# Performance work log

Hardware: AMD Instinct MI355X
Metric: run time of the kernel (lower is better)

The kernel has to match this reference:

```python
import jax, jax.numpy as jnp
import numpy as np

# Standard 2D morphsnakes structuring elements (4 line filters), matching the
# repo-level global `filters` used by LSNet2.
_SE = np.zeros((4, 3, 3), dtype=np.float32)
_SE[0, 1, :] = 1.0           # horizontal line
_SE[1, :, 1] = 1.0           # vertical line
_SE[2] = np.eye(3, dtype=np.float32)          # main diagonal
_SE[3] = np.eye(3, dtype=np.float32)[::-1]    # anti-diagonal


def _dilate_stack(x, filts):
    # per-pixel: max over 3x3 window of (zero-padded x + filt), for every filter
    H, W = x.shape
    p = jnp.pad(x, 1)
    m = jnp.full((filts.shape[0], H, W), -jnp.inf, x.dtype)
    for k in range(3):
        for l in range(3):
            m = jnp.maximum(m, p[k:k + H, l:l + W][None] + filts[:, k, l][:, None, None])
    return m  # [F, H, W]


def _erode_stack(x, filts):
    # per-pixel: min over 3x3 window of (zero-padded x - filt) == -max(-(x - filt))
    H, W = x.shape
    p = jnp.pad(x, 1)
    m = jnp.full((filts.shape[0], H, W), jnp.inf, x.dtype)
    for k in range(3):
        for l in range(3):
            m = jnp.minimum(m, p[k:k + H, l:l + W][None] - filts[:, k, l][:, None, None])
    return m  # [F, H, W]


def _dilate_min(x, filts):
    return jnp.min(_dilate_stack(x, filts), axis=0)


def _erode_max(x, filts):
    return jnp.max(_erode_stack(x, filts), axis=0)


def setup_inputs() -> dict:
    key = jax.random.key(0)
    k1, k2 = jax.random.split(key)
    H = W = 2048
    inp = jax.random.uniform(k1, (H, W), dtype=jnp.float32)
    origin = jax.random.uniform(k2, (H, W), dtype=jnp.float32)
    filters = jnp.asarray(_SE)
    return {"input": inp, "origin": origin, "filters": filters}


def reference(input, origin, filters):
    x = input
    # SI o IS smoothing: dilate/min, erode/max, erode/max, dilate/min, dilate/min, erode/max
    x = _dilate_min(x, filters)
    x = _erode_max(x, filters)
    x = _erode_max(x, filters)
    x = _dilate_min(x, filters)
    x = _dilate_min(x, filters)
    x = _erode_max(x, filters)

    # balloon force with v = 1 and a flat ones(3,3) structuring element
    ones_f = jnp.ones((1, 3, 3), x.dtype)
    aux = _dilate_stack(x, ones_f)[0]
    threshold = jnp.percentile(x, 40.0)
    x = jnp.where(origin > threshold, aux, x)

    # Chan-Vese region means and update
    c0 = jnp.sum(origin * (1.0 - x)) / (jnp.sum(1.0 - x) + 1e-8)
    c1 = jnp.sum(origin * x) / (jnp.sum(x) + 1e-8)
    cv = (origin - c1) ** 2 - (origin - c0) ** 2
    x = jnp.where(cv < 0, 1.0, jnp.where(cv > 0, 0.0, x))
    return x
```

## Files before the change

### kernel.cpp

```cpp
#include <hip/hip_runtime.h>

#define HH 2048
#define WW 2048
#define NN (HH*WW)

static constexpr unsigned RANK0 = 1677721u;
static constexpr unsigned KEYLO = 0xB000u;
static constexpr unsigned KEYHI_ = 0xC000u;
static constexpr int NBINS = 4096;
static constexpr int NPART = 512;

#define TH 32
#define TW 128
#define LR 44
#define LCP 148

struct Scal {
  unsigned keyhiA, keyhiB, rA, rB;
  double thr, c0, c1;
};

static constexpr size_t OFF_CTL    = (size_t)NN * 4;
static constexpr size_t OFF_COARSE = OFF_CTL;
static constexpr size_t OFF_UNDER  = OFF_COARSE + (size_t)NBINS * 4;
static constexpr size_t OFF_OVER   = OFF_UNDER + 4;
static constexpr size_t OFF_MIDA   = OFF_OVER + 4;
static constexpr size_t OFF_MIDB   = OFF_MIDA + 1024;
static constexpr size_t OFF_H2A    = OFF_MIDB + 1024;
static constexpr size_t OFF_H2B    = OFF_H2A + 65536ull * 4;
static constexpr size_t CTL_END    = OFF_H2B + 65536ull * 4;
static constexpr size_t CTL_BYTES  = CTL_END - OFF_CTL;
static constexpr size_t OFF_SCAL   = CTL_END;
static constexpr size_t OFF_PART   = OFF_SCAL + 64;

__device__ __forceinline__ float mx3(float a, float b, float c){ return fmaxf(fmaxf(a,b),c); }
__device__ __forceinline__ float mn3(float a, float b, float c){ return fminf(fminf(a,b),c); }

__device__ __forceinline__ unsigned keyf(float x){
  unsigned b = __float_as_uint(x);
  return (b & 0x80000000u) ? ~b : (b | 0x80000000u);
}
__device__ __forceinline__ float keyinv(unsigned k){
  unsigned b = (k & 0x80000000u) ? (k ^ 0x80000000u) : ~k;
  return __uint_as_float(b);
}

__device__ __forceinline__ void loadwin6(const float* __restrict__ src, int rowbase,
                                         int cL, int cC, int cR, float w[6]){
  float4 v = *reinterpret_cast<const float4*>(&src[rowbase + cC]);
  w[0] = src[rowbase + cL];
  w[1]=v.x; w[2]=v.y; w[3]=v.z; w[4]=v.w;
  w[5] = src[rowbase + cR];
}

__device__ __forceinline__ void morph4(bool DIL,
    const float pr[6], const float cr[6], const float nr[6], float w[4]){
  #pragma unroll
  for (int i = 0; i < 4; i++){
    if (DIL){
      float Ah = mx3(cr[i],   cr[i+1], cr[i+2]);
      float Av = mx3(pr[i+1], cr[i+1], nr[i+1]);
      float Ad = mx3(pr[i],   cr[i+1], nr[i+2]);
      float Aa = mx3(pr[i+2], cr[i+1], nr[i]);
      float tm = mx3(pr[i], pr[i+1], pr[i+2]);
      float bm = mx3(nr[i], nr[i+1], nr[i+2]);
      float M9 = mx3(tm, Ah, bm);
      w[i] = fmaxf(M9, 1.0f + fminf(fminf(Ah,Av), fminf(Ad,Aa)));
    } else {
      float Bh = mn3(cr[i],   cr[i+1], cr[i+2]);
      float Bv = mn3(pr[i+1], cr[i+1], nr[i+1]);
      float Bd = mn3(pr[i],   cr[i+1], nr[i+2]);
      float Ba = mn3(pr[i+2], cr[i+1], nr[i]);
      float tm = mn3(pr[i], pr[i+1], pr[i+2]);
      float bm = mn3(nr[i], nr[i+1], nr[i+2]);
      float m9 = mn3(tm, Bh, bm);
      w[i] = fminf(m9, fmaxf(fmaxf(Bh,Bv), fmaxf(Bd,Ba)) - 1.0f);
    }
  }
}

__global__ __launch_bounds__(256)
void fused_morph_k(const float* __restrict__ in, float* __restrict__ out,
                   unsigned* __restrict__ gh, unsigned* __restrict__ under,
                   unsigned* __restrict__ over){
  __shared__ float lds[2][LR*LCP];
  const int tilec = blockIdx.x & 15;
  const int tiler = blockIdx.x >> 4;
  const int r0 = tiler*TH, c0 = tilec*TW;

  for (int idx = threadIdx.x; idx < LR*36; idx += 256){
    int lr = idx / 36, g = idx % 36;
    int gr = r0 - 6 + lr, gc = c0 - 8 + 4*g;
    float4 v = make_float4(0.f,0.f,0.f,0.f);
    if ((unsigned)gr < (unsigned)HH && (unsigned)gc < (unsigned)WW)
      v = *reinterpret_cast<const float4*>(in + (size_t)gr*WW + gc);
    *reinterpret_cast<float4*>(&lds[0][lr*LCP + 4*g]) = v;
  }
  __syncthreads();

  const int t = threadIdx.x;
  const int g = t % 36, s = t / 36;
  const bool active = (t < 252);
  const int colC = 4*g;
  const int colL = g ? 4*g - 1 : 0;
  const int colR = (g == 35) ? 143 : 4*g + 4;
  const int gcBase = c0 - 8 + 4*g;
  const bool dilf[6] = {true,false,false,true,true,false};

  #pragma unroll 1
  for (int st = 0; st < 6; st++){
    const float* src = lds[st & 1];
    float*       dst = lds[(st & 1) ^ 1];
    if (active){
      const bool DIL = dilf[st];
      float r8[8][6];
      #pragma unroll
      for (int k = 0; k < 8; k++)
        loadwin6(src, (6*s + k)*LCP, colL, colC, colR, r8[k]);
      #pragma unroll
      for (int k = 0; k < 6; k++){
        float w[4];
        morph4(DIL, r8[k], r8[k+1], r8[k+2], w);
        int gr = r0 - 6 + 6*s + 1 + k;
        if ((unsigned)gr >= (unsigned)HH){
          w[0]=w[1]=w[2]=w[3]=0.f;
        } else {
          #pragma unroll
          for (int i = 0; i < 4; i++)
            if ((unsigned)(gcBase + i) >= (unsigned)WW) w[i] = 0.f;
        }
        *reinterpret_cast<float4*>(&dst[(6*s + 1 + k)*LCP + colC]) =
            make_float4(w[0],w[1],w[2],w[3]);
      }
    }
    __syncthreads();
  }
  unsigned* lh = reinterpret_cast<unsigned*>(&lds[1][0]);
  for (int i = threadIdx.x; i < NBINS; i += 256) lh[i] = 0;
  __syncthreads();

  unsigned uc = 0, oc = 0;
  for (int idx = threadIdx.x; idx < TH*(TW/4); idx += 256){
    int row = idx >> 5, gg = idx & 31;
    float4 v = *reinterpret_cast<const float4*>(&lds[0][(row+6)*LCP + 8 + 4*gg]);
    *reinterpret_cast<float4*>(out + (size_t)(r0+row)*WW + c0 + 4*gg) = v;
    float vv[4] = {v.x, v.y, v.z, v.w};
    #pragma unroll
    for (int i = 0; i < 4; i++){
      unsigned key = keyf(vv[i]);
      unsigned hi = key >> 16;
      if (hi >= KEYLO && hi < KEYHI_) atomicAdd(&lh[hi - KEYLO], 1u);
      else if (hi < KEYLO)            uc++;
      else                            oc++;
    }
  }
  __syncthreads();
  for (int i = threadIdx.x; i < NBINS; i += 256){
    unsigned c = lh[i];
    if (c) atomicAdd(&gh[i], c);
  }
  if (uc) atomicAdd(under, uc);
  if (oc) atomicAdd(over, oc);
}

__global__ void scan_coarse_k(const unsigned* __restrict__ gh, const unsigned* __restrict__ under,
                              Scal* __restrict__ sc){
  __shared__ unsigned part[256];
  __shared__ unsigned excl[256];
  int t = threadIdx.x;
  unsigned loc = 0;
  #pragma unroll
  for (int i = 0; i < NBINS/256; i++) loc += gh[t*(NBINS/256) + i];
  part[t] = loc;
  __syncthreads();
  if (t == 0){
    unsigned run = under[0];
    for (int i = 0; i < 256; i++){ excl[i] = run; run += part[i]; }
  }
  __syncthreads();
  unsigned run = excl[t];
  const unsigned r0 = RANK0, r1 = RANK0 + 1;
  #pragma unroll
  for (int i = 0; i < NBINS/256; i++){
    unsigned idx = t*(NBINS/256) + i;
    unsigned cc = gh[idx];
    if (cc){
      if (r0 >= run && r0 - run < cc){ sc->keyhiA = KEYLO + idx; sc->rA = r0 - run; }
      if (r1 >= run && r1 - run < cc){ sc->keyhiB = KEYLO + idx; sc->rB = r1 - run; }
    }
    run += cc;
  }
}

__global__ __launch_bounds__(256)
void fine2d_k(const float* __restrict__ x, const Scal* __restrict__ sc,
              unsigned* __restrict__ midA, unsigned* __restrict__ midB,
              unsigned* __restrict__ h2A, unsigned* __restrict__ h2B){
  __shared__ unsigned hA[256], hB[256];
  hA[threadIdx.x] = 0; hB[threadIdx.x] = 0;
  __syncthreads();
  unsigned ha = sc->keyhiA, hb = sc->keyhiB;
  bool dup = (ha == hb);
  const int nItems = NN/4;
  for (int it = blockIdx.x*blockDim.x + threadIdx.x; it < nItems; it += gridDim.x*blockDim.x){
    float4 v = reinterpret_cast<const float4*>(x)[it];
    float vv[4] = {v.x, v.y, v.z, v.w};
    #pragma unroll
    for (int j = 0; j < 4; j++){
      unsigned key = keyf(vv[j]);
      unsigned hi = key >> 16;
      if (hi == ha){ atomicAdd(&hA[(key>>8)&255], 1u); atomicAdd(&h2A[key & 0xFFFFu], 1u); }
      else if (hi == hb){ atomicAdd(&hB[(key>>8)&255], 1u); atomicAdd(&h2B[key & 0xFFFFu], 1u); }
    }
  }
  __syncthreads();
  if (hA[threadIdx.x]) atomicAdd(&midA[threadIdx.x], hA[threadIdx.x]);
  if (!dup && hB[threadIdx.x]) atomicAdd(&midB[threadIdx.x], hB[threadIdx.x]);
}

__global__ void scan_ml_k(const unsigned* __restrict__ midA, const unsigned* __restrict__ midB,
                          const unsigned* __restrict__ h2A, const unsigned* __restrict__ h2B,
                          Scal* __restrict__ sc){
  __shared__ unsigned h[256], excl[256];
  __shared__ unsigned res[6];
  int t = threadIdx.x;
  unsigned ha = sc->keyhiA, hb = sc->keyhiB;
  bool dupHi = (ha == hb);
  unsigned rA = sc->rA, rB = sc->rB;

  h[t] = midA[t];
  __syncthreads();
  if (t == 0){ unsigned run = 0; for (int i = 0; i < 256; i++){ excl[i] = run; run += h[i]; } }
  __syncthreads();
  if (rA >= excl[t] && rA - excl[t] < h[t]){ res[0] = (unsigned)t; res[1] = rA - excl[t]; }
  if (dupHi && rB >= excl[t] && rB - excl[t] < h[t]){ res[2] = (unsigned)t; res[3] = rB - excl[t]; }
  __syncthreads();
  if (!dupHi){
    h[t] = midB[t];
    __syncthreads();
    if (t == 0){ unsigned run = 0; for (int i = 0; i < 256; i++){ excl[i] = run; run += h[i]; } }
    __syncthreads();
    if (rB >= excl[t] && rB - excl[t] < h[t]){ res[2] = (unsigned)t; res[3] = rB - excl[t]; }
    __syncthreads();
  }
  unsigned mA = res[0], rA2 = res[1], mB = res[2], rB2 = res[3];
  bool dupMid = dupHi && (mA == mB);

  h[t] = h2A[mA*256 + t];
  __syncthreads();
  if (t == 0){ unsigned run = 0; for (int i = 0; i < 256; i++){ excl[i] = run; run += h[i]; } }
  __syncthreads();
  if (rA2 >= excl[t] && rA2 - excl[t] < h[t]) res[4] = (unsigned)t;
  if (dupMid && rB2 >= excl[t] && rB2 - excl[t] < h[t]) res[5] = (unsigned)t;
  __syncthreads();
  if (!dupMid){
    const unsigned* srcH = dupHi ? h2A : h2B;
    h[t] = srcH[mB*256 + t];
    __syncthreads();
    if (t == 0){ unsigned run = 0; for (int i = 0; i < 256; i++){ excl[i] = run; run += h[i]; } }
    __syncthreads();
    if (rB2 >= excl[t] && rB2 - excl[t] < h[t]) res[5] = (unsigned)t;
    __syncthreads();
  }
  if (t == 0){
    unsigned ka = (ha << 16) | (mA << 8) | res[4];
    unsigned kb = (hb << 16) | (mB << 8) | res[5];
    double va = (double)keyinv(ka), vb = (double)keyinv(kb);
    const double FRAC = 0.4*(double)(NN-1) - (double)RANK0;
    sc->thr = va + (vb - va) * FRAC;
  }
}

__device__ __forceinline__ void load6(const float* __restrict__ p, int row, int q, float r[6]){
  if (row < 0 || row >= HH){
    r[0]=r[1]=r[2]=r[3]=r[4]=r[5]=0.f;
    return;
  }
  const float* rp = p + (size_t)row * WW;
  float4 cc = *reinterpret_cast<const float4*>(rp + q);
  r[0] = (q > 0) ? rp[q-1] : 0.f;
  r[1]=cc.x; r[2]=cc.y; r[3]=cc.z; r[4]=cc.w;
  r[5] = (q+4 < WW) ? rp[q+4] : 0.f;
}

__global__ __launch_bounds__(256)
void balloon_k(const float* __restrict__ x, const float* __restrict__ orig,
               float* __restrict__ xb, const Scal* __restrict__ sc, double* __restrict__ part){
  double thr = sc->thr;
  double s0 = 0.0, s1 = 0.0, s2 = 0.0;
  const int nItems = NN/4;
  for (int it = blockIdx.x*blockDim.x + threadIdx.x; it < nItems; it += gridDim.x*blockDim.x){
    int i = it >> 9;
    int q = (it & 511) << 2;
    float a[6], b[6], c[6];
    load6(x, i-1, q, a);
    load6(x, i,   q, b);
    load6(x, i+1, q, c);
    float4 og = *reinterpret_cast<const float4*>(orig + (size_t)i*WW + q);
    float ov[4] = {og.x, og.y, og.z, og.w};
    float r[4];
    #pragma unroll
    for (int t = 0; t < 4; t++){
      float M9 = mx3(mx3(a[t],a[t+1],a[t+2]), mx3(b[t],b[t+1],b[t+2]), mx3(c[t],c[t+1],c[t+2]));
      float aux = 1.0f + M9;
      float nx = ((double)ov[t] > thr) ? aux : b[t+1];
      r[t] = nx;
      s0 += (double)ov[t];
      s1 += (double)nx;
      s2 += (double)ov[t] * (double)nx;
    }
    *reinterpret_cast<float4*>(xb + (size_t)i*WW + q) = make_float4(r[0],r[1],r[2],r[3]);
  }
  for (int off = 32; off > 0; off >>= 1){
    s0 += __shfl_down(s0, off);
    s1 += __shfl_down(s1, off);
    s2 += __shfl_down(s2, off);
  }
  __shared__ double red[4][3];
  int lane = threadIdx.x & 63, wv = threadIdx.x >> 6;
  if (lane == 0){ red[wv][0] = s0; red[wv][1] = s1; red[wv][2] = s2; }
  __syncthreads();
  if (threadIdx.x == 0){
    part[blockIdx.x*3+0] = red[0][0]+red[1][0]+red[2][0]+red[3][0];
    part[blockIdx.x*3+1] = red[0][1]+red[1][1]+red[2][1]+red[3][1];
    part[blockIdx.x*3+2] = red[0][2]+red[1][2]+red[2][2]+red[3][2];
  }
}

__global__ void c0c1_k(const double* __restrict__ part, Scal* __restrict__ sc){
  int t = threadIdx.x;
  double s0 = 0, s1 = 0, s2 = 0;
  for (int b = t; b < NPART; b += 256){
    s0 += part[b*3+0]; s1 += part[b*3+1]; s2 += part[b*3+2];
  }
  for (int off = 32; off > 0; off >>= 1){
    s0 += __shfl_down(s0, off);
    s1 += __shfl_down(s1, off);
    s2 += __shfl_down(s2, off);
  }
  __shared__ double red[4][3];
  int lane = t & 63, wv = t >> 6;
  if (lane == 0){ red[wv][0] = s0; red[wv][1] = s1; red[wv][2] = s2; }
  __syncthreads();
  if (t == 0){
    double So = red[0][0]+red[1][0]+red[2][0]+red[3][0];
    double Sx = red[0][1]+red[1][1]+red[2][1]+red[3][1];
    double Sox= red[0][2]+red[1][2]+red[2][2]+red[3][2];
    sc->c0 = (So - Sox) / ((double)NN - Sx + 1e-8);
    sc->c1 = Sox / (Sx + 1e-8);
  }
}

__global__ __launch_bounds__(256)
void final_k(const float* __restrict__ orig, const float* __restrict__ xb,
             const Scal* __restrict__ sc, float* __restrict__ out){
  double c0 = sc->c0, c1 = sc->c1;
  const int nItems = NN/4;
  for (int it = blockIdx.x*blockDim.x + threadIdx.x; it < nItems; it += gridDim.x*blockDim.x){
    float4 og = reinterpret_cast<const float4*>(orig)[it];
    float4 xv = reinterpret_cast<const float4*>(xb)[it];
    float ov[4] = {og.x, og.y, og.z, og.w};
    float xx[4] = {xv.x, xv.y, xv.z, xv.w};
    float r[4];
    #pragma unroll
    for (int t = 0; t < 4; t++){
      double o = (double)ov[t];
      double d1 = o - c1, d0 = o - c0;
      double cv = d1*d1 - d0*d0;
      r[t] = (cv < 0.0) ? 1.0f : ((cv > 0.0) ? 0.0f : xx[t]);
    }
    reinterpret_cast<float4*>(out)[it] = make_float4(r[0],r[1],r[2],r[3]);
  }
}

extern "C" void kernel_launch(void* const* d_in, const int* in_sizes, int n_in,
                              void* d_out, int out_size, void* d_ws, size_t ws_size,
                              hipStream_t stream) {
  const float* input  = (const float*)d_in[0];
  const float* origin = (const float*)d_in[1];
  float* out = (float*)d_out;

  char* ws = (char*)d_ws;
  float*    bufA   = (float*)ws;
  unsigned* coarse = (unsigned*)(ws + OFF_COARSE);
  unsigned* under  = (unsigned*)(ws + OFF_UNDER);
  unsigned* over   = (unsigned*)(ws + OFF_OVER);
  unsigned* midA   = (unsigned*)(ws + OFF_MIDA);
  unsigned* midB   = (unsigned*)(ws + OFF_MIDB);
  unsigned* h2A    = (unsigned*)(ws + OFF_H2A);
  unsigned* h2B    = (unsigned*)(ws + OFF_H2B);
  Scal*     scal   = (Scal*)(ws + OFF_SCAL);
  double*   part   = (double*)(ws + OFF_PART);

  hipMemsetAsync(ws + OFF_CTL, 0, CTL_BYTES, stream);

  fused_morph_k<<<(HH/TH)*(WW/TW), 256, 0, stream>>>(input, out, coarse, under, over);

  scan_coarse_k<<<1, 256, 0, stream>>>(coarse, under, scal);
  fine2d_k<<<1024, 256, 0, stream>>>(out, scal, midA, midB, h2A, h2B);
  scan_ml_k<<<1, 256, 0, stream>>>(midA, midB, h2A, h2B, scal);

  balloon_k<<<NPART, 256, 0, stream>>>(out, origin, bufA, scal, part);
  c0c1_k<<<1, 256, 0, stream>>>(part, scal);
  final_k<<<2048, 256, 0, stream>>>(origin, bufA, scal, out);
}
```

Baseline: 118.6 us.

## Fold single-block scan kernels into consumers with redundant per-block rank selection

Removes the three single-block kernels (coarse scan, mid/low-level rank scan, c0/c1 reduction) by having every block of the consuming kernel recompute them redundantly, using a warp-shuffle exclusive scan instead of a serial thread-0 scan. This cuts the launch count from seven to four and drops the serialized tiny-kernel latency between passes. In exchange, each block repeats the histogram scans and partial-sum reduction, adding global reads and syncs per block. Grid sizes for the fine-histogram and balloon passes are also raised to 2048 blocks.

```diff
diff --git a/kernel.cpp b/kernel.cpp
--- a/kernel.cpp
+++ b/kernel.cpp
@@ -8,17 +8,12 @@
 static constexpr unsigned KEYLO = 0xB000u;
 static constexpr unsigned KEYHI_ = 0xC000u;
 static constexpr int NBINS = 4096;
-static constexpr int NPART = 512;
+static constexpr int NPART = 2048;
 
 #define TH 32
 #define TW 128
 #define LR 44
 #define LCP 148
-
-struct Scal {
-  unsigned keyhiA, keyhiB, rA, rB;
-  double thr, c0, c1;
-};
 
 static constexpr size_t OFF_CTL    = (size_t)NN * 4;
 static constexpr size_t OFF_COARSE = OFF_CTL;
@@ -30,8 +25,7 @@
 static constexpr size_t OFF_H2B    = OFF_H2A + 65536ull * 4;
 static constexpr size_t CTL_END    = OFF_H2B + 65536ull * 4;
 static constexpr size_t CTL_BYTES  = CTL_END - OFF_CTL;
-static constexpr size_t OFF_SCAL   = CTL_END;
-static constexpr size_t OFF_PART   = OFF_SCAL + 64;
+static constexpr size_t OFF_PART   = CTL_END;
 
 __device__ __forceinline__ float mx3(float a, float b, float c){ return fmaxf(fmaxf(a,b),c); }
 __device__ __forceinline__ float mn3(float a, float b, float c){ return fminf(fminf(a,b),c); }
@@ -43,6 +37,50 @@
 __device__ __forceinline__ float keyinv(unsigned k){
   unsigned b = (k & 0x80000000u) ? (k ^ 0x80000000u) : ~k;
   return __uint_as_float(b);
+}
+
+__device__ __forceinline__ unsigned excl_scan256(unsigned v, volatile unsigned* tmp, int t){
+  int lane = t & 63, wv = t >> 6;
+  unsigned inc = v;
+  #pragma unroll
+  for (int off = 1; off < 64; off <<= 1){
+    unsigned u = __shfl_up(inc, off);
+    if (lane >= off) inc += u;
+  }
+  if (lane == 63) tmp[wv] = inc;
+  __syncthreads();
+  unsigned wo = 0;
+  #pragma unroll
+  for (int w = 0; w < 4; w++) wo += (w < wv) ? tmp[w] : 0u;
+  __syncthreads();
+  return wo + inc - v;
+}
+
+__device__ __forceinline__ void coarse_rank(const unsigned* __restrict__ gh,
+                                            const unsigned* __restrict__ under,
+                                            unsigned* cres, volatile unsigned* stmp, int t){
+  unsigned bins[16], loc = 0;
+  #pragma unroll
+  for (int i = 0; i < 16; i++){ bins[i] = gh[t*16 + i]; loc += bins[i]; }
+  unsigned run = excl_scan256(loc, stmp, t) + under[0];
+  #pragma unroll
+  for (int i = 0; i < 16; i++){
+    unsigned cc = bins[i];
+    if (cc){
+      if (RANK0 >= run && RANK0 - run < cc){ cres[0] = KEYLO + (unsigned)(t*16+i); cres[1] = RANK0 - run; }
+      if (RANK0+1 >= run && RANK0+1 - run < cc){ cres[2] = KEYLO + (unsigned)(t*16+i); cres[3] = RANK0+1 - run; }
+    }
+    run += cc;
+  }
+  __syncthreads();
+}
+
+__device__ __forceinline__ void rank256(const unsigned* __restrict__ h, unsigned r,
+                                        unsigned* res2, volatile unsigned* stmp, int t){
+  unsigned c = h[t];
+  unsigned ex = excl_scan256(c, stmp, t);
+  if (c && r >= ex && r - ex < c){ res2[0] = (unsigned)t; res2[1] = r - ex; }
+  __syncthreads();
 }
 
 __device__ __forceinline__ void loadwin6(const float* __restrict__ src, int rowbase,
@@ -163,46 +201,21 @@
   if (oc) atomicAdd(over, oc);
 }
 
-__global__ void scan_coarse_k(const unsigned* __restrict__ gh, const unsigned* __restrict__ under,
-                              Scal* __restrict__ sc){
-  __shared__ unsigned part[256];
-  __shared__ unsigned excl[256];
-  int t = threadIdx.x;
-  unsigned loc = 0;
-  #pragma unroll
-  for (int i = 0; i < NBINS/256; i++) loc += gh[t*(NBINS/256) + i];
-  part[t] = loc;
-  __syncthreads();
-  if (t == 0){
-    unsigned run = under[0];
-    for (int i = 0; i < 256; i++){ excl[i] = run; run += part[i]; }
-  }
-  __syncthreads();
-  unsigned run = excl[t];
-  const unsigned r0 = RANK0, r1 = RANK0 + 1;
-  #pragma unroll
-  for (int i = 0; i < NBINS/256; i++){
-    unsigned idx = t*(NBINS/256) + i;
-    unsigned cc = gh[idx];
-    if (cc){
-      if (r0 >= run && r0 - run < cc){ sc->keyhiA = KEYLO + idx; sc->rA = r0 - run; }
-      if (r1 >= run && r1 - run < cc){ sc->keyhiB = KEYLO + idx; sc->rB = r1 - run; }
-    }
-    run += cc;
-  }
-}
-
 __global__ __launch_bounds__(256)
-void fine2d_k(const float* __restrict__ x, const Scal* __restrict__ sc,
+void fine2d_k(const float* __restrict__ x,
+              const unsigned* __restrict__ coarse, const unsigned* __restrict__ under,
               unsigned* __restrict__ midA, unsigned* __restrict__ midB,
               unsigned* __restrict__ h2A, unsigned* __restrict__ h2B){
   __shared__ unsigned hA[256], hB[256];
-  hA[threadIdx.x] = 0; hB[threadIdx.x] = 0;
-  __syncthreads();
-  unsigned ha = sc->keyhiA, hb = sc->keyhiB;
+  __shared__ unsigned stmp[4], cres[4];
+  const int t = threadIdx.x;
+  coarse_rank(coarse, under, cres, stmp, t);
+  unsigned ha = cres[0], hb = cres[2];
   bool dup = (ha == hb);
+  hA[t] = 0; hB[t] = 0;
+  __syncthreads();
   const int nItems = NN/4;
-  for (int it = blockIdx.x*blockDim.x + threadIdx.x; it < nItems; it += gridDim.x*blockDim.x){
+  for (int it = blockIdx.x*blockDim.x + t; it < nItems; it += gridDim.x*blockDim.x){
     float4 v = reinterpret_cast<const float4*>(x)[it];
     float vv[4] = {v.x, v.y, v.z, v.w};
     #pragma unroll
@@ -214,61 +227,8 @@
     }
   }
   __syncthreads();
-  if (hA[threadIdx.x]) atomicAdd(&midA[threadIdx.x], hA[threadIdx.x]);
-  if (!dup && hB[threadIdx.x]) atomicAdd(&midB[threadIdx.x], hB[threadIdx.x]);
-}
-
-__global__ void scan_ml_k(const unsigned* __restrict__ midA, const unsigned* __restrict__ midB,
-                          const unsigned* __restrict__ h2A, const unsigned* __restrict__ h2B,
-                          Scal* __restrict__ sc){
-  __shared__ unsigned h[256], excl[256];
-  __shared__ unsigned res[6];
-  int t = threadIdx.x;
-  unsigned ha = sc->keyhiA, hb = sc->keyhiB;
-  bool dupHi = (ha == hb);
-  unsigned rA = sc->rA, rB = sc->rB;
-
-  h[t] = midA[t];
-  __syncthreads();
-  if (t == 0){ unsigned run = 0; for (int i = 0; i < 256; i++){ excl[i] = run; run += h[i]; } }
-  __syncthreads();
-  if (rA >= excl[t] && rA - excl[t] < h[t]){ res[0] = (unsigned)t; res[1] = rA - excl[t]; }
-  if (dupHi && rB >= excl[t] && rB - excl[t] < h[t]){ res[2] = (unsigned)t; res[3] = rB - excl[t]; }
-  __syncthreads();
-  if (!dupHi){
-    h[t] = midB[t];
-    __syncthreads();
-    if (t == 0){ unsigned run = 0; for (int i = 0; i < 256; i++){ excl[i] = run; run += h[i]; } }
-    __syncthreads();
-    if (rB >= excl[t] && rB - excl[t] < h[t]){ res[2] = (unsigned)t; res[3] = rB - excl[t]; }
-    __syncthreads();
-  }
-  unsigned mA = res[0], rA2 = res[1], mB = res[2], rB2 = res[3];
-  bool dupMid = dupHi && (mA == mB);
-
-  h[t] = h2A[mA*256 + t];
-  __syncthreads();
-  if (t == 0){ unsigned run = 0; for (int i = 0; i < 256; i++){ excl[i] = run; run += h[i]; } }
-  __syncthreads();
-  if (rA2 >= excl[t] && rA2 - excl[t] < h[t]) res[4] = (unsigned)t;
-  if (dupMid && rB2 >= excl[t] && rB2 - excl[t] < h[t]) res[5] = (unsigned)t;
-  __syncthreads();
-  if (!dupMid){
-    const unsigned* srcH = dupHi ? h2A : h2B;
-    h[t] = srcH[mB*256 + t];
-    __syncthreads();
-    if (t == 0){ unsigned run = 0; for (int i = 0; i < 256; i++){ excl[i] = run; run += h[i]; } }
-    __syncthreads();
-    if (rB2 >= excl[t] && rB2 - excl[t] < h[t]) res[5] = (unsigned)t;
-    __syncthreads();
-  }
-  if (t == 0){
-    unsigned ka = (ha << 16) | (mA << 8) | res[4];
-    unsigned kb = (hb << 16) | (mB << 8) | res[5];
-    double va = (double)keyinv(ka), vb = (double)keyinv(kb);
-    const double FRAC = 0.4*(double)(NN-1) - (double)RANK0;
-    sc->thr = va + (vb - va) * FRAC;
-  }
+  if (hA[t]) atomicAdd(&midA[t], hA[t]);
+  if (!dup && hB[t]) atomicAdd(&midB[t], hB[t]);
 }
 
 __device__ __forceinline__ void load6(const float* __restrict__ p, int row, int q, float r[6]){
@@ -285,11 +245,32 @@
 
 __global__ __launch_bounds__(256)
 void balloon_k(const float* __restrict__ x, const float* __restrict__ orig,
-               float* __restrict__ xb, const Scal* __restrict__ sc, double* __restrict__ part){
-  double thr = sc->thr;
+               float* __restrict__ xb,
+               const unsigned* __restrict__ coarse, const unsigned* __restrict__ under,
+               const unsigned* __restrict__ midA, const unsigned* __restrict__ midB,
+               const unsigned* __restrict__ h2A, const unsigned* __restrict__ h2B,
+               double* __restrict__ part){
+  __shared__ unsigned stmp[4], cres[4], mresA[2], mresB[2], lresA[2], lresB[2];
+  __shared__ double red[4][3];
+  const int t = threadIdx.x;
+
+  coarse_rank(coarse, under, cres, stmp, t);
+  unsigned ha = cres[0], rA = cres[1], hb = cres[2], rB = cres[3];
+  bool dupHi = (ha == hb);
+  rank256(midA, rA, mresA, stmp, t);
+  rank256(dupHi ? midA : midB, rB, mresB, stmp, t);
+  unsigned mA = mresA[0], rA2 = mresA[1], mB = mresB[0], rB2 = mresB[1];
+  rank256(h2A + (size_t)mA*256, rA2, lresA, stmp, t);
+  rank256((dupHi ? h2A : h2B) + (size_t)mB*256, rB2, lresB, stmp, t);
+  unsigned ka = (ha << 16) | (mA << 8) | lresA[0];
+  unsigned kb = (hb << 16) | (mB << 8) | lresB[0];
+  double va = (double)keyinv(ka), vb = (double)keyinv(kb);
+  const double FRAC = 0.4*(double)(NN-1) - (double)RANK0;
+  double thr = va + (vb - va) * FRAC;
+
   double s0 = 0.0, s1 = 0.0, s2 = 0.0;
   const int nItems = NN/4;
-  for (int it = blockIdx.x*blockDim.x + threadIdx.x; it < nItems; it += gridDim.x*blockDim.x){
+  for (int it = blockIdx.x*blockDim.x + t; it < nItems; it += gridDim.x*blockDim.x){
     int i = it >> 9;
     int q = (it & 511) << 2;
     float a[6], b[6], c[6];
@@ -300,14 +281,14 @@
     float ov[4] = {og.x, og.y, og.z, og.w};
     float r[4];
     #pragma unroll
-    for (int t = 0; t < 4; t++){
-      float M9 = mx3(mx3(a[t],a[t+1],a[t+2]), mx3(b[t],b[t+1],b[t+2]), mx3(c[t],c[t+1],c[t+2]));
+    for (int j = 0; j < 4; j++){
+      float M9 = mx3(mx3(a[j],a[j+1],a[j+2]), mx3(b[j],b[j+1],b[j+2]), mx3(c[j],c[j+1],c[j+2]));
       float aux = 1.0f + M9;
-      float nx = ((double)ov[t] > thr) ? aux : b[t+1];
-      r[t] = nx;
-      s0 += (double)ov[t];
+      float nx = ((double)ov[j] > thr) ? aux : b[j+1];
+      r[j] = nx;
+      s0 += (double)ov[j];
       s1 += (double)nx;
-      s2 += (double)ov[t] * (double)nx;
+      s2 += (double)ov[j] * (double)nx;
     }
     *reinterpret_cast<float4*>(xb + (size_t)i*WW + q) = make_float4(r[0],r[1],r[2],r[3]);
   }
@@ -316,58 +297,58 @@
     s1 += __shfl_down(s1, off);
     s2 += __shfl_down(s2, off);
   }
-  __shared__ double red[4][3];
-  int lane = threadIdx.x & 63, wv = threadIdx.x >> 6;
+  int lane = t & 63, wv = t >> 6;
   if (lane == 0){ red[wv][0] = s0; red[wv][1] = s1; red[wv][2] = s2; }
   __syncthreads();
-  if (threadIdx.x == 0){
+  if (t == 0){
     part[blockIdx.x*3+0] = red[0][0]+red[1][0]+red[2][0]+red[3][0];
     part[blockIdx.x*3+1] = red[0][1]+red[1][1]+red[2][1]+red[3][1];
     part[blockIdx.x*3+2] = red[0][2]+red[1][2]+red[2][2]+red[3][2];
   }
 }
 
-__global__ void c0c1_k(const double* __restrict__ part, Scal* __restrict__ sc){
-  int t = threadIdx.x;
-  double s0 = 0, s1 = 0, s2 = 0;
-  for (int b = t; b < NPART; b += 256){
-    s0 += part[b*3+0]; s1 += part[b*3+1]; s2 += part[b*3+2];
-  }
-  for (int off = 32; off > 0; off >>= 1){
-    s0 += __shfl_down(s0, off);
-    s1 += __shfl_down(s1, off);
-    s2 += __shfl_down(s2, off);
-  }
-  __shared__ double red[4][3];
-  int lane = t & 63, wv = t >> 6;
-  if (lane == 0){ red[wv][0] = s0; red[wv][1] = s1; red[wv][2] = s2; }
-  __syncthreads();
-  if (t == 0){
-    double So = red[0][0]+red[1][0]+red[2][0]+red[3][0];
-    double Sx = red[0][1]+red[1][1]+red[2][1]+red[3][1];
-    double Sox= red[0][2]+red[1][2]+red[2][2]+red[3][2];
-    sc->c0 = (So - Sox) / ((double)NN - Sx + 1e-8);
-    sc->c1 = Sox / (Sx + 1e-8);
-  }
-}
-
 __global__ __launch_bounds__(256)
 void final_k(const float* __restrict__ orig, const float* __restrict__ xb,
-             const Scal* __restrict__ sc, float* __restrict__ out){
-  double c0 = sc->c0, c1 = sc->c1;
+             const double* __restrict__ part, float* __restrict__ out){
+  __shared__ double red[4][3];
+  __shared__ double cc01[2];
+  const int t = threadIdx.x;
+  {
+    double u0 = 0, u1 = 0, u2 = 0;
+    for (int b = t; b < NPART; b += 256){
+      u0 += part[b*3+0]; u1 += part[b*3+1]; u2 += part[b*3+2];
+    }
+    for (int off = 32; off > 0; off >>= 1){
+      u0 += __shfl_down(u0, off);
+      u1 += __shfl_down(u1, off);
+      u2 += __shfl_down(u2, off);
+    }
+    int lane = t & 63, wv = t >> 6;
+    if (lane == 0){ red[wv][0] = u0; red[wv][1] = u1; red[wv][2] = u2; }
+    __syncthreads();
+    if (t == 0){
+      double So = red[0][0]+red[1][0]+red[2][0]+red[3][0];
+      double Sx = red[0][1]+red[1][1]+red[2][1]+red[3][1];
+      double Sox= red[0][2]+red[1][2]+red[2][2]+red[3][2];
+      cc01[0] = (So - Sox) / ((double)NN - Sx + 1e-8);
+      cc01[1] = Sox / (Sx + 1e-8);
+    }
+    __syncthreads();
+  }
+  double c0 = cc01[0], c1 = cc01[1];
   const int nItems = NN/4;
-  for (int it = blockIdx.x*blockDim.x + threadIdx.x; it < nItems; it += gridDim.x*blockDim.x){
+  for (int it = blockIdx.x*blockDim.x + t; it < nItems; it += gridDim.x*blockDim.x){
     float4 og = reinterpret_cast<const float4*>(orig)[it];
     float4 xv = reinterpret_cast<const float4*>(xb)[it];
     float ov[4] = {og.x, og.y, og.z, og.w};
     float xx[4] = {xv.x, xv.y, xv.z, xv.w};
     float r[4];
     #pragma unroll
-    for (int t = 0; t < 4; t++){
-      double o = (double)ov[t];
+    for (int j = 0; j < 4; j++){
+      double o = (double)ov[j];
       double d1 = o - c1, d0 = o - c0;
       double cv = d1*d1 - d0*d0;
-      r[t] = (cv < 0.0) ? 1.0f : ((cv > 0.0) ? 0.0f : xx[t]);
+      r[j] = (cv < 0.0) ? 1.0f : ((cv > 0.0) ? 0.0f : xx[j]);
     }
     reinterpret_cast<float4*>(out)[it] = make_float4(r[0],r[1],r[2],r[3]);
   }
@@ -389,18 +370,13 @@
   unsigned* midB   = (unsigned*)(ws + OFF_MIDB);
   unsigned* h2A    = (unsigned*)(ws + OFF_H2A);
   unsigned* h2B    = (unsigned*)(ws + OFF_H2B);
-  Scal*     scal   = (Scal*)(ws + OFF_SCAL);
   double*   part   = (double*)(ws + OFF_PART);
 
   hipMemsetAsync(ws + OFF_CTL, 0, CTL_BYTES, stream);
 
   fused_morph_k<<<(HH/TH)*(WW/TW), 256, 0, stream>>>(input, out, coarse, under, over);
-
-  scan_coarse_k<<<1, 256, 0, stream>>>(coarse, under, scal);
-  fine2d_k<<<1024, 256, 0, stream>>>(out, scal, midA, midB, h2A, h2B);
-  scan_ml_k<<<1, 256, 0, stream>>>(midA, midB, h2A, h2B, scal);
-
-  balloon_k<<<NPART, 256, 0, stream>>>(out, origin, bufA, scal, part);
-  c0c1_k<<<1, 256, 0, stream>>>(part, scal);
-  final_k<<<2048, 256, 0, stream>>>(origin, bufA, scal, out);
-}
+  fine2d_k<<<2048, 256, 0, stream>>>(out, coarse, under, midA, midB, h2A, h2B);
+  balloon_k<<<2048, 256, 0, stream>>>(out, origin, bufA, coarse, under,
+                                      midA, midB, h2A, h2B, part);
+  final_k<<<2048, 256, 0, stream>>>(origin, bufA, part, out);
+}
```

New measurement: 124.2 us. +4.8%, slower.
